# Kernel tuning notes

Hardware: AMD Instinct MI355X
Metric: run time of the kernel (lower is better)

The kernel has to match this reference:

```python
import jax, jax.numpy as jnp
import numpy as np

# ---- geometry / config constants (from init_kwargs: MandoFanBeamConfig) ----
DET = 816          # detEltCount == sgmWidth
VIEWS = 720        # sgmHeight == views
DU = 1.0           # detEltSize [mm]
OFF = 0.0          # detOffCenter [mm]
SID = 750.0        # source-isocenter distance [mm]
SDD = 1250.0       # source-detector distance [mm]
IMG = 512          # imgDim
PIX = 0.5          # pixelSize [mm]
TOTAL = 2.0 * np.pi  # totalScanAngle = 360 deg
START = 0.0        # startAngle


def make_ramp_filter(N, du):
    # zxInitRampFilter: discrete ramp (Ram-Lak) kernel, center at N//2 - 1
    n = np.arange(N)
    center = N // 2 - 1
    d = n - center
    f = np.zeros(N, dtype=np.float32)
    odd = (d % 2) != 0
    f[odd] = -1.0 / (np.pi * d[odd] * du) ** 2
    f[center] = 1.0 / (2.0 * du) ** 2
    return f


def setup_inputs() -> dict:
    key = jax.random.key(0)
    x = jax.random.normal(key, (8, VIEWS, DET), dtype=jnp.float32)
    filt = jnp.asarray(make_ramp_filter(DET, DU))
    return {"x": x, "filt": filt}


def _filter_sinogram(x, filt):
    # zxFilterSinogram: per-row conv1d with padding='same', then * du.
    # Vectorized: fold (B, H) into the conv batch dim instead of a python loop.
    B, H, W = x.shape
    k = filt.shape[0]
    lhs = x.reshape(B * H, 1, W)                 # (N, C=1, W)
    rhs = filt.reshape(1, 1, k)                  # (O=1, I=1, K) cross-correlation, like torch
    pad = ((k - 1) // 2, k // 2)                 # torch 'same' asymmetric padding for even k
    y = jax.lax.conv_general_dilated(lhs, rhs, window_strides=(1,), padding=[pad])
    return y.reshape(B, H, W) * DU


def _backproject(sgm):
    # Fan-beam FBP backprojection, flat detector, equivalent math to the
    # torch_mando_cuda.backward kernel with KERNEL_NONE (filtering already done).
    B = sgm.shape[0]
    dbeta = TOTAL / VIEWS
    betas = START + jnp.arange(VIEWS, dtype=jnp.float32) * dbeta

    c = (jnp.arange(IMG, dtype=jnp.float32) - (IMG - 1) / 2.0) * PIX
    X, Y = jnp.meshgrid(c, -c)                   # (IMG, IMG); image y axis points up

    # cosine pre-weighting of the (filtered) sinogram: sid / sqrt(sid^2 + u^2)
    u_det = (jnp.arange(DET, dtype=jnp.float32) - (DET - 1) / 2.0) * DU + OFF
    cosw = SID / jnp.sqrt(SID * SID + u_det * u_det)
    sgm_w = sgm * cosw                           # (B, VIEWS, DET)

    def body(img, inp):
        beta, row = inp                          # row: (B, DET)
        cb, sb = jnp.cos(beta), jnp.sin(beta)
        xr = X * cb + Y * sb                     # pixel coords in rotated frame
        yr = -X * sb + Y * cb
        L = SID - yr                             # source-to-pixel distance along central ray
        u = SDD * xr / L                         # detector coordinate hit by this pixel's ray
        w = (SID * SID) / (L * L)                # fan-beam distance weight
        t = (u - OFF) / DU + (DET - 1) / 2.0     # fractional detector index
        i0 = jnp.clip(jnp.floor(t).astype(jnp.int32), 0, DET - 2)
        frac = t - i0.astype(jnp.float32)
        v0 = row[:, i0]                          # (B, IMG, IMG) gather
        v1 = row[:, i0 + 1]
        val = v0 * (1.0 - frac) + v1 * frac      # linear interpolation
        inside = (t >= 0.0) & (t <= DET - 1)
        img = img + jnp.where(inside, w * val, 0.0)
        return img, None

    init = jnp.zeros((B, IMG, IMG), dtype=sgm.dtype)
    img, _ = jax.lax.scan(body, init, (betas, jnp.swapaxes(sgm_w, 0, 1)))
    return img * dbeta


def reference(x, filt):
    x = _filter_sinogram(x, filt)
    return _backproject(x)
```

## Files before the change

### kernel.cpp

```cpp
#include <hip/hip_runtime.h>
#include <math.h>

namespace {
constexpr int DETN = 816;
constexpr int NVIEW = 720;
constexpr int NB = 8;
constexpr int IMGN = 512;
constexpr float PIXSZ = 0.5f;
constexpr float SID = 750.0f;
constexpr float SDD = 1250.0f;
constexpr float DBETA = 6.28318530717958647692f / 720.0f;

constexpr int XPAD = 1632;
constexpr int T = 16;
constexpr int TPR = DETN / T;
constexpr int ROWSTRIDE = 1736;
constexpr int NBB = 4;

constexpr int NSPLIT = 2;
constexpr int VH = NVIEW / NSPLIT;
constexpr int VP = VH / 2;

typedef _Float16 h2 __attribute__((ext_vector_type(2)));
typedef float f2 __attribute__((ext_vector_type(2)));

__device__ __forceinline__ int skew(int i) { return i + (i >> 4); }
__device__ __forceinline__ f2 fma2(f2 a, f2 b, f2 c) {
  return __builtin_elementwise_fma(a, b, c);
}
__device__ __forceinline__ h2 pack_h2(float a, float b) {
  return __builtin_bit_cast(h2, __builtin_amdgcn_cvt_pkrtz(a, b));
}

__global__ __launch_bounds__(256) void filt_kernel(
    const float* __restrict__ x, const float* __restrict__ filt,
    h2* __restrict__ sino2)
{
  __shared__ float xs[NBB * ROWSTRIDE];
  const int tid = threadIdx.x;
  const int v = blockIdx.x >> 1;
  const int bhalf = blockIdx.x & 1;

  for (int p = tid; p < NBB * XPAD; p += 256) {
    int b = p / XPAD;
    int q = p - b * XPAD;
    int src = q - 407;
    float val = 0.0f;
    if (src >= 0 && src < DETN)
      val = x[((bhalf * NBB + b) * NVIEW + v) * DETN + src];
    xs[b * ROWSTRIDE + skew(q)] = val;
  }
  __syncthreads();

  const bool active = tid < NBB * TPR;
  const int b = tid / TPR;
  const int t = tid - b * TPR;
  const int w0 = t * T;
  f2 acc2[8];

  if (active) {
    const float* __restrict__ xrow = &xs[b * ROWSTRIDE];
    f2 p[8];
#pragma unroll
    for (int k = 0; k < 8; ++k) {
      p[k].x = xrow[skew(w0 + k)];
      p[k].y = xrow[skew(w0 + k + 8)];
      acc2[k] = (f2){0.0f, 0.0f};
    }

    for (int s8 = 0; s8 < 51; ++s8) {
#pragma unroll
      for (int u = 0; u < 8; ++u) {
        const int s = s8 * 8 + u;
        const float fv = filt[2 * s];
        const f2 fv2 = {fv, fv};
#pragma unroll
        for (int k = 0; k < 8; ++k) {
          const int idx = (2 * u + k) & 15;
          const f2 v2 = (idx < 8)
              ? p[idx]
              : __builtin_shufflevector(p[idx - 8], p[idx - 8], 1, 0);
          acc2[k] = fma2(v2, fv2, acc2[k]);
        }
        const float nv0 = xrow[skew(w0 + 2 * s + 16)];
        const float nv1 = xrow[skew(w0 + 2 * s + 17)];
        if (2 * u < 8) p[2 * u].x = nv0; else p[2 * u - 8].y = nv0;
        if (2 * u + 1 < 8) p[2 * u + 1].x = nv1; else p[2 * u - 7].y = nv1;
      }
    }
    const float fc = filt[407];
    const f2 fc2 = {fc, fc};
#pragma unroll
    for (int k = 0; k < 8; ++k) {
      f2 v2;
      v2.x = xrow[skew(w0 + k + 407)];
      v2.y = xrow[skew(w0 + k + 415)];
      acc2[k] = fma2(v2, fc2, acc2[k]);
    }
#pragma unroll
    for (int k = 0; k < 8; ++k) {
      const float udx = (float)(w0 + k) - 407.5f;
      const float udy = (float)(w0 + k + 8) - 407.5f;
      acc2[k].x *= SID / sqrtf(SID * SID + udx * udx);
      acc2[k].y *= SID / sqrtf(SID * SID + udy * udy);
    }
  }
  __syncthreads();

  float* ys = xs;
  if (active) {
#pragma unroll
    for (int k = 0; k < 8; ++k) {
      ys[b * (DETN + 1) + w0 + k] = acc2[k].x;
      ys[b * (DETN + 1) + w0 + k + 8] = acc2[k].y;
    }
    if (t == 0) ys[b * (DETN + 1) + DETN] = 0.0f;
  }
  __syncthreads();

  h2* dst = sino2 + (size_t)v * DETN * NB + bhalf * NBB;
  for (int idx = tid; idx < DETN * NBB; idx += 256) {
    const int w = idx >> 2;
    const int bb = idx & 3;
    h2 hp;
    hp[0] = (_Float16)ys[bb * (DETN + 1) + w];
    hp[1] = (_Float16)ys[bb * (DETN + 1) + w + 1];
    dst[w * 8 + bb] = hp;
  }
}

__device__ __forceinline__ float dot2acc(h2 w, unsigned int q, float acc) {
  return __builtin_amdgcn_fdot2(w, __builtin_bit_cast(h2, q), acc, false);
}

__global__ __launch_bounds__(1024, 2) void bp_kernel(
    const h2* __restrict__ sino2, float* __restrict__ out)
{
  __shared__ f2 cbp_t[VP], sbp_t[VP], csp_t[VP], ssp_t[VP];
  const int tid = threadIdx.x;
  const int v0 = blockIdx.z * VH;
  for (int it = tid; it < VP; it += 1024) {
    float sA, cA, sB, cB;
    sincosf((float)(v0 + 2 * it) * DBETA, &sA, &cA);
    sincosf((float)(v0 + 2 * it + 1) * DBETA, &sB, &cB);
    cbp_t[it] = (f2){cA, cB};
    sbp_t[it] = (f2){sA, sB};
    csp_t[it] = (f2){SDD * cA, SDD * cB};
    ssp_t[it] = (f2){SDD * sA, SDD * sB};
  }
  __syncthreads();

  const int lane = tid & 63;
  const int wv = tid >> 6;
  const int px = ((wv & 3) << 3) | (lane & 7);
  const int py = ((wv >> 2) << 3) | (lane >> 3);
  const int j = (blockIdx.x << 5) + px;
  const int i = (blockIdx.y << 5) + py;
  const float X = ((float)j - 255.5f) * PIXSZ;
  const float Y = -(((float)i - 255.5f) * PIXSZ);
  const f2 X2 = {X, X};
  const f2 Y2 = {Y, Y};
  const f2 nY2 = {-Y, -Y};
  const f2 SID2 = {SID, SID};
  const f2 C4075 = {407.5f, 407.5f};

  float acc[NB];
#pragma unroll
  for (int b = 0; b < NB; ++b) acc[b] = 0.0f;

  const char* pv = (const char*)sino2 + (size_t)v0 * DETN * NB * 4;
  constexpr int VSTRIDE = DETN * NB * 4;

  for (int it = 0; it < VP; ++it) {
    const f2 cbp = cbp_t[it];
    const f2 sbp = sbp_t[it];
    const f2 csp = csp_t[it];
    const f2 ssp = ssp_t[it];

    const f2 num = fma2(Y2, ssp, X2 * csp);
    const f2 L = fma2(nY2, cbp, fma2(X2, sbp, SID2));
    const float rA = __builtin_amdgcn_rcpf(L.x);
    const float rB = __builtin_amdgcn_rcpf(L.y);
    const f2 rL = {rA, rB};
    const f2 tt = fma2(num, rL, C4075);
    const f2 m = SID2 * rL;
    const f2 w = m * m;
    const float i0fA = floorf(tt.x);
    const float i0fB = floorf(tt.y);
    const int i0A = (int)i0fA;
    const int i0B = (int)i0fB;
    const f2 frac = tt - (f2){i0fA, i0fB};
    const f2 a1 = w * frac;
    const f2 a0 = w - a1;
    const h2 wpA = pack_h2(a0.x, a1.x);
    const h2 wpB = pack_h2(a0.y, a1.y);

    const uint4* pA = (const uint4*)(pv + (i0A << 5));
    const uint4* pB = (const uint4*)(pv + VSTRIDE + (i0B << 5));
    const uint4 qA0 = pA[0];
    const uint4 qA1 = pA[1];
    const uint4 qB0 = pB[0];
    const uint4 qB1 = pB[1];

    acc[0] = dot2acc(wpA, qA0.x, acc[0]);
    acc[1] = dot2acc(wpA, qA0.y, acc[1]);
    acc[2] = dot2acc(wpA, qA0.z, acc[2]);
    acc[3] = dot2acc(wpA, qA0.w, acc[3]);
    acc[4] = dot2acc(wpA, qA1.x, acc[4]);
    acc[5] = dot2acc(wpA, qA1.y, acc[5]);
    acc[6] = dot2acc(wpA, qA1.z, acc[6]);
    acc[7] = dot2acc(wpA, qA1.w, acc[7]);

    acc[0] = dot2acc(wpB, qB0.x, acc[0]);
    acc[1] = dot2acc(wpB, qB0.y, acc[1]);
    acc[2] = dot2acc(wpB, qB0.z, acc[2]);
    acc[3] = dot2acc(wpB, qB0.w, acc[3]);
    acc[4] = dot2acc(wpB, qB1.x, acc[4]);
    acc[5] = dot2acc(wpB, qB1.y, acc[5]);
    acc[6] = dot2acc(wpB, qB1.z, acc[6]);
    acc[7] = dot2acc(wpB, qB1.w, acc[7]);

    pv += 2 * VSTRIDE;
  }

#pragma unroll
  for (int b = 0; b < NB; ++b)
    atomicAdd(&out[(b * IMGN + i) * IMGN + j], acc[b] * DBETA);
}

}

extern "C" void kernel_launch(void* const* d_in, const int* in_sizes, int n_in,
                              void* d_out, int out_size, void* d_ws, size_t ws_size,
                              hipStream_t stream) {
  const float* x = (const float*)d_in[0];
  const float* filt = (const float*)d_in[1];
  float* out = (float*)d_out;
  h2* sino2 = (h2*)d_ws;

  (void)hipMemsetAsync(out, 0, (size_t)out_size * sizeof(float), stream);
  filt_kernel<<<NVIEW * 2, 256, 0, stream>>>(x, filt, sino2);
  bp_kernel<<<dim3(IMGN / 32, IMGN / 32, NSPLIT), 1024, 0, stream>>>(sino2, out);
}
```

Measured before the change: 269.9 us.

## Shrink backprojection blocks, unroll four views per iteration, repack filter pairs

The backprojection kernel moves from 32x32 pixel blocks of 1024 threads to 16x16 blocks of 256 threads with a 6-block occupancy hint. Its view loop now processes four views per iteration so more sinogram loads are in flight at once. The filter kernel switches to an interleaved output ownership (each thread handles adjacent pixel pairs) with a new shared-memory skew, allowing 8-byte vector LDS loads and a simpler rotating register window. The extra unrolling raises register pressure, and the smaller blocks cost more sincos table setup across blocks.

```diff
diff --git a/kernel.cpp b/kernel.cpp
--- a/kernel.cpp
+++ b/kernel.cpp
@@ -14,17 +14,20 @@
 constexpr int XPAD = 1632;
 constexpr int T = 16;
 constexpr int TPR = DETN / T;
-constexpr int ROWSTRIDE = 1736;
+constexpr int ROWSTRIDE = 1840;
 constexpr int NBB = 4;
 
 constexpr int NSPLIT = 2;
 constexpr int VH = NVIEW / NSPLIT;
 constexpr int VP = VH / 2;
+constexpr int VQ = VH / 4;
 
 typedef _Float16 h2 __attribute__((ext_vector_type(2)));
 typedef float f2 __attribute__((ext_vector_type(2)));
 
-__device__ __forceinline__ int skew(int i) { return i + (i >> 4); }
+__device__ __forceinline__ int F(int i) { return i + 2 * (i >> 4); }
+__device__ __forceinline__ int pairF(int pp) { return 2 * pp + 2 * (pp >> 3); }
+
 __device__ __forceinline__ f2 fma2(f2 a, f2 b, f2 c) {
   return __builtin_elementwise_fma(a, b, c);
 }
@@ -43,12 +46,12 @@
 
   for (int p = tid; p < NBB * XPAD; p += 256) {
     int b = p / XPAD;
-    int q = p - b * XPAD;
-    int src = q - 407;
+    int qq = p - b * XPAD;
+    int src = qq - 407;
     float val = 0.0f;
     if (src >= 0 && src < DETN)
       val = x[((bhalf * NBB + b) * NVIEW + v) * DETN + src];
-    xs[b * ROWSTRIDE + skew(q)] = val;
+    xs[b * ROWSTRIDE + F(qq)] = val;
   }
   __syncthreads();
 
@@ -60,11 +63,11 @@
 
   if (active) {
     const float* __restrict__ xrow = &xs[b * ROWSTRIDE];
-    f2 p[8];
-#pragma unroll
-    for (int k = 0; k < 8; ++k) {
-      p[k].x = xrow[skew(w0 + k)];
-      p[k].y = xrow[skew(w0 + k + 8)];
+    const int P0 = 8 * t;
+    f2 q[8];
+#pragma unroll
+    for (int k = 0; k < 8; ++k) {
+      q[k] = *(const f2*)&xrow[pairF(P0 + k)];
       acc2[k] = (f2){0.0f, 0.0f};
     }
 
@@ -75,32 +78,21 @@
         const float fv = filt[2 * s];
         const f2 fv2 = {fv, fv};
 #pragma unroll
-        for (int k = 0; k < 8; ++k) {
-          const int idx = (2 * u + k) & 15;
-          const f2 v2 = (idx < 8)
-              ? p[idx]
-              : __builtin_shufflevector(p[idx - 8], p[idx - 8], 1, 0);
-          acc2[k] = fma2(v2, fv2, acc2[k]);
-        }
-        const float nv0 = xrow[skew(w0 + 2 * s + 16)];
-        const float nv1 = xrow[skew(w0 + 2 * s + 17)];
-        if (2 * u < 8) p[2 * u].x = nv0; else p[2 * u - 8].y = nv0;
-        if (2 * u + 1 < 8) p[2 * u + 1].x = nv1; else p[2 * u - 7].y = nv1;
+        for (int k = 0; k < 8; ++k)
+          acc2[k] = fma2(q[(u + k) & 7], fv2, acc2[k]);
+        q[u & 7] = *(const f2*)&xrow[pairF(P0 + s + 8)];
       }
     }
     const float fc = filt[407];
-    const f2 fc2 = {fc, fc};
-#pragma unroll
-    for (int k = 0; k < 8; ++k) {
-      f2 v2;
-      v2.x = xrow[skew(w0 + k + 407)];
-      v2.y = xrow[skew(w0 + k + 415)];
-      acc2[k] = fma2(v2, fc2, acc2[k]);
-    }
-#pragma unroll
-    for (int k = 0; k < 8; ++k) {
-      const float udx = (float)(w0 + k) - 407.5f;
-      const float udy = (float)(w0 + k + 8) - 407.5f;
+#pragma unroll
+    for (int k = 0; k < 8; ++k) {
+      acc2[k].x = fmaf(xrow[F(w0 + 2 * k + 407)], fc, acc2[k].x);
+      acc2[k].y = fmaf(xrow[F(w0 + 2 * k + 408)], fc, acc2[k].y);
+    }
+#pragma unroll
+    for (int k = 0; k < 8; ++k) {
+      const float udx = (float)(w0 + 2 * k) - 407.5f;
+      const float udy = (float)(w0 + 2 * k + 1) - 407.5f;
       acc2[k].x *= SID / sqrtf(SID * SID + udx * udx);
       acc2[k].y *= SID / sqrtf(SID * SID + udy * udy);
     }
@@ -111,8 +103,8 @@
   if (active) {
 #pragma unroll
     for (int k = 0; k < 8; ++k) {
-      ys[b * (DETN + 1) + w0 + k] = acc2[k].x;
-      ys[b * (DETN + 1) + w0 + k + 8] = acc2[k].y;
+      ys[b * (DETN + 1) + w0 + 2 * k] = acc2[k].x;
+      ys[b * (DETN + 1) + w0 + 2 * k + 1] = acc2[k].y;
     }
     if (t == 0) ys[b * (DETN + 1) + DETN] = 0.0f;
   }
@@ -133,13 +125,13 @@
   return __builtin_amdgcn_fdot2(w, __builtin_bit_cast(h2, q), acc, false);
 }
 
-__global__ __launch_bounds__(1024, 2) void bp_kernel(
+__global__ __launch_bounds__(256, 6) void bp_kernel(
     const h2* __restrict__ sino2, float* __restrict__ out)
 {
   __shared__ f2 cbp_t[VP], sbp_t[VP], csp_t[VP], ssp_t[VP];
   const int tid = threadIdx.x;
   const int v0 = blockIdx.z * VH;
-  for (int it = tid; it < VP; it += 1024) {
+  for (int it = tid; it < VP; it += 256) {
     float sA, cA, sB, cB;
     sincosf((float)(v0 + 2 * it) * DBETA, &sA, &cA);
     sincosf((float)(v0 + 2 * it + 1) * DBETA, &sB, &cB);
@@ -152,10 +144,10 @@
 
   const int lane = tid & 63;
   const int wv = tid >> 6;
-  const int px = ((wv & 3) << 3) | (lane & 7);
-  const int py = ((wv >> 2) << 3) | (lane >> 3);
-  const int j = (blockIdx.x << 5) + px;
-  const int i = (blockIdx.y << 5) + py;
+  const int px = ((wv & 1) << 3) | (lane & 7);
+  const int py = ((wv >> 1) << 3) | (lane >> 3);
+  const int j = (blockIdx.x << 4) + px;
+  const int i = (blockIdx.y << 4) + py;
   const float X = ((float)j - 255.5f) * PIXSZ;
   const float Y = -(((float)i - 255.5f) * PIXSZ);
   const f2 X2 = {X, X};
@@ -171,36 +163,42 @@
   const char* pv = (const char*)sino2 + (size_t)v0 * DETN * NB * 4;
   constexpr int VSTRIDE = DETN * NB * 4;
 
-  for (int it = 0; it < VP; ++it) {
-    const f2 cbp = cbp_t[it];
-    const f2 sbp = sbp_t[it];
-    const f2 csp = csp_t[it];
-    const f2 ssp = ssp_t[it];
-
-    const f2 num = fma2(Y2, ssp, X2 * csp);
-    const f2 L = fma2(nY2, cbp, fma2(X2, sbp, SID2));
-    const float rA = __builtin_amdgcn_rcpf(L.x);
-    const float rB = __builtin_amdgcn_rcpf(L.y);
-    const f2 rL = {rA, rB};
-    const f2 tt = fma2(num, rL, C4075);
-    const f2 m = SID2 * rL;
-    const f2 w = m * m;
-    const float i0fA = floorf(tt.x);
-    const float i0fB = floorf(tt.y);
-    const int i0A = (int)i0fA;
-    const int i0B = (int)i0fB;
-    const f2 frac = tt - (f2){i0fA, i0fB};
-    const f2 a1 = w * frac;
-    const f2 a0 = w - a1;
-    const h2 wpA = pack_h2(a0.x, a1.x);
-    const h2 wpB = pack_h2(a0.y, a1.y);
+  for (int qd = 0; qd < VQ; ++qd) {
+    const f2 cb0 = cbp_t[2 * qd],     cb1 = cbp_t[2 * qd + 1];
+    const f2 sb0 = sbp_t[2 * qd],     sb1 = sbp_t[2 * qd + 1];
+    const f2 cs0 = csp_t[2 * qd],     cs1 = csp_t[2 * qd + 1];
+    const f2 ss0 = ssp_t[2 * qd],     ss1 = ssp_t[2 * qd + 1];
+
+    const f2 num0 = fma2(Y2, ss0, X2 * cs0);
+    const f2 num1 = fma2(Y2, ss1, X2 * cs1);
+    const f2 L0 = fma2(nY2, cb0, fma2(X2, sb0, SID2));
+    const f2 L1 = fma2(nY2, cb1, fma2(X2, sb1, SID2));
+    const f2 rL0 = {__builtin_amdgcn_rcpf(L0.x), __builtin_amdgcn_rcpf(L0.y)};
+    const f2 rL1 = {__builtin_amdgcn_rcpf(L1.x), __builtin_amdgcn_rcpf(L1.y)};
+    const f2 tt0 = fma2(num0, rL0, C4075);
+    const f2 tt1 = fma2(num1, rL1, C4075);
+    const f2 m0 = SID2 * rL0, m1 = SID2 * rL1;
+    const f2 w0 = m0 * m0, w1 = m1 * m1;
+    const float iA = floorf(tt0.x), iB = floorf(tt0.y);
+    const float iC = floorf(tt1.x), iD = floorf(tt1.y);
+    const int i0A = (int)iA, i0B = (int)iB, i0C = (int)iC, i0D = (int)iD;
+    const f2 fr0 = tt0 - (f2){iA, iB};
+    const f2 fr1 = tt1 - (f2){iC, iD};
+    const f2 a1p0 = w0 * fr0, a1p1 = w1 * fr1;
+    const f2 a0p0 = w0 - a1p0, a0p1 = w1 - a1p1;
+    const h2 wpA = pack_h2(a0p0.x, a1p0.x);
+    const h2 wpB = pack_h2(a0p0.y, a1p0.y);
+    const h2 wpC = pack_h2(a0p1.x, a1p1.x);
+    const h2 wpD = pack_h2(a0p1.y, a1p1.y);
 
     const uint4* pA = (const uint4*)(pv + (i0A << 5));
     const uint4* pB = (const uint4*)(pv + VSTRIDE + (i0B << 5));
-    const uint4 qA0 = pA[0];
-    const uint4 qA1 = pA[1];
-    const uint4 qB0 = pB[0];
-    const uint4 qB1 = pB[1];
+    const uint4* pC = (const uint4*)(pv + 2 * VSTRIDE + (i0C << 5));
+    const uint4* pD = (const uint4*)(pv + 3 * VSTRIDE + (i0D << 5));
+    const uint4 qA0 = pA[0], qA1 = pA[1];
+    const uint4 qB0 = pB[0], qB1 = pB[1];
+    const uint4 qC0 = pC[0], qC1 = pC[1];
+    const uint4 qD0 = pD[0], qD1 = pD[1];
 
     acc[0] = dot2acc(wpA, qA0.x, acc[0]);
     acc[1] = dot2acc(wpA, qA0.y, acc[1]);
@@ -220,7 +218,25 @@
     acc[6] = dot2acc(wpB, qB1.z, acc[6]);
     acc[7] = dot2acc(wpB, qB1.w, acc[7]);
 
-    pv += 2 * VSTRIDE;
+    acc[0] = dot2acc(wpC, qC0.x, acc[0]);
+    acc[1] = dot2acc(wpC, qC0.y, acc[1]);
+    acc[2] = dot2acc(wpC, qC0.z, acc[2]);
+    acc[3] = dot2acc(wpC, qC0.w, acc[3]);
+    acc[4] = dot2acc(wpC, qC1.x, acc[4]);
+    acc[5] = dot2acc(wpC, qC1.y, acc[5]);
+    acc[6] = dot2acc(wpC, qC1.z, acc[6]);
+    acc[7] = dot2acc(wpC, qC1.w, acc[7]);
+
+    acc[0] = dot2acc(wpD, qD0.x, acc[0]);
+    acc[1] = dot2acc(wpD, qD0.y, acc[1]);
+    acc[2] = dot2acc(wpD, qD0.z, acc[2]);
+    acc[3] = dot2acc(wpD, qD0.w, acc[3]);
+    acc[4] = dot2acc(wpD, qD1.x, acc[4]);
+    acc[5] = dot2acc(wpD, qD1.y, acc[5]);
+    acc[6] = dot2acc(wpD, qD1.z, acc[6]);
+    acc[7] = dot2acc(wpD, qD1.w, acc[7]);
+
+    pv += 4 * VSTRIDE;
   }
 
 #pragma unroll
@@ -240,5 +256,5 @@
 
   (void)hipMemsetAsync(out, 0, (size_t)out_size * sizeof(float), stream);
   filt_kernel<<<NVIEW * 2, 256, 0, stream>>>(x, filt, sino2);
-  bp_kernel<<<dim3(IMGN / 32, IMGN / 32, NSPLIT), 1024, 0, stream>>>(sino2, out);
-}
+  bp_kernel<<<dim3(IMGN / 16, IMGN / 16, NSPLIT), 256, 0, stream>>>(sino2, out);
+}
```

Result: faster. 254.2 us (-5.8%).
